# Kernel optimization log

Measured on AMD Instinct MI355X. Metric: run time of the kernel, lower is better.

Reference implementation:

```python
import jax, jax.numpy as jnp
import numpy as np

B, T, M, C, H = 4, 2048, 256, 512, 8
D = C // H  # head dim = 64


def _split_heads(t, n):  # [B,N,C] -> [B,H,N,D]
    b, s, c = t.shape
    return t.reshape(b, s, H, c // H).transpose(0, 2, 1, 3)


def setup_inputs() -> dict:
    key = jax.random.key(0)
    ks = jax.random.split(key, 16)
    s = 0.02
    inp = {
        "x": jax.random.normal(ks[0], (B, T, C), jnp.float32),
        "y": jax.random.normal(ks[1], (B, M, C), jnp.float32),
        "attn_x_mask": jnp.tril(jnp.ones((T, T), jnp.int32))[None, None],  # causal [1,1,T,T]
        "Wqkv_x": jax.random.normal(ks[2], (C, 3 * C), jnp.float32) * s,
        "bqkv_x": jnp.zeros((3 * C,), jnp.float32),
        "Wqkv_y": jax.random.normal(ks[3], (C, 3 * C), jnp.float32) * s,
        "bqkv_y": jnp.zeros((3 * C,), jnp.float32),
        "Wgs": jax.random.normal(ks[4], (C, C), jnp.float32) * s,
        "bgs": jnp.zeros((C,), jnp.float32),
        "Wgc": jax.random.normal(ks[5], (C, C), jnp.float32) * s,
        "bgc": jnp.zeros((C,), jnp.float32),
        "Wp": jax.random.normal(ks[6], (C, C), jnp.float32) * s,
        "bp": jnp.zeros((C,), jnp.float32),
    }
    return inp


def reference(x, y, attn_x_mask, Wqkv_x, bqkv_x, Wqkv_y, bqkv_y, Wgs, bgs, Wgc, bgc, Wp, bp):
    b, t, c = x.shape
    _, m, _ = y.shape
    scale = 1.0 / np.sqrt(D).astype(np.float32)

    qx, kx, vx = jnp.split(x @ Wqkv_x + bqkv_x, 3, axis=-1)
    qy, ky, vy = jnp.split(y @ Wqkv_y + bqkv_y, 3, axis=-1)
    qx, kx, vx = _split_heads(qx, H), _split_heads(kx, H), _split_heads(vx, H)
    qy, ky, vy = _split_heads(qy, H), _split_heads(ky, H), _split_heads(vy, H)

    # self-attn logits over x: [B,H,T,T]
    satt = jnp.einsum('bhtd,bhsd->bhts', qx, kx) * scale
    # cross scores y->x: [B,H,M,T]; bias = mean over M of softmax(dim=M)*scores -> [B,H,1,T]
    catt_y = jnp.einsum('bhmd,bhtd->bhmt', qy, kx) * scale
    bias = jnp.mean(jax.nn.softmax(catt_y, axis=-2) * catt_y, axis=-2, keepdims=True)
    satt = satt + bias  # broadcast over query rows
    satt = jnp.where(attn_x_mask == 0, -jnp.inf, satt)
    satt = jax.nn.softmax(satt, axis=-1)

    # cross-attn x->y: [B,H,T,M]
    catt = jax.nn.softmax(jnp.einsum('bhtd,bhmd->bhtm', qx, ky) * scale, axis=-1)

    sval = jnp.einsum('bhts,bhsd->bhtd', satt, vx).transpose(0, 2, 1, 3).reshape(b, t, c)
    cval = jnp.einsum('bhtm,bhmd->bhtd', catt, vy).transpose(0, 2, 1, 3).reshape(b, t, c)

    sgate = jax.nn.sigmoid(sval @ Wgs + bgs)
    cgate = jax.nn.sigmoid(cval @ Wgc + bgc)
    out = (sgate * cval + cgate * sval) @ Wp + bp
    return out
```

## Files before the change

### kernel.cpp

```cpp
#include <hip/hip_runtime.h>
#include <hip/hip_bf16.h>
#include <math.h>

#define B_ 4
#define T_ 2048
#define M_ 256
#define C_ 512
#define H_ 8
#define D_ 64
#define TC3 1536
#define QSCALE2 0.18033688f

typedef _Float16 half_t;
typedef _Float16 half8 __attribute__((ext_vector_type(8)));
typedef _Float16 half4 __attribute__((ext_vector_type(4)));
typedef float floatx4 __attribute__((ext_vector_type(4)));

__device__ __forceinline__ void gload_lds16(const half_t* g, half_t* lds) {
  __builtin_amdgcn_global_load_lds(
      (const __attribute__((address_space(1))) unsigned int*)g,
      (__attribute__((address_space(3))) unsigned int*)(unsigned)(unsigned long long)(void*)lds,
      16, 0, 0);
}

__device__ __forceinline__ floatx4 mfma16(half8 a, half8 b, floatx4 c) {
  return __builtin_amdgcn_mfma_f32_16x16x32_f16(a, b, c, 0, 0, 0);
}
__device__ __forceinline__ floatx4 mfma16k16(half4 a, half4 b, floatx4 c) {
  return __builtin_amdgcn_mfma_f32_16x16x16f16(a, b, c, 0, 0, 0);
}

__device__ __forceinline__ half8 frag64(const half_t* lds, int row, int kc, int quad) {
  int slot = ((kc << 2) + quad) ^ (row & 7);
  return *(const half8*)(lds + row * 64 + slot * 8);
}

__global__ __launch_bounds__(256) void conv_all(
    const float* x, half_t* xo, const float* y, half_t* yo,
    const float* w0, const float* w1, const float* w2, const float* w3, const float* w4,
    half_t* o0, half_t* o1, half_t* o2, half_t* o3, half_t* o4) {
  __shared__ float tile[32][33];
  const int tid = threadIdx.x;
  if (blockIdx.x < 2304) {
    int blk = blockIdx.x;
    const float* src; half_t* dst; int N;
    if (blk < 768)       { src = w0; dst = o0; N = 1536; }
    else if (blk < 1536) { src = w1; dst = o1; N = 1536; blk -= 768; }
    else if (blk < 1792) { src = w2; dst = o2; N = 512;  blk -= 1536; }
    else if (blk < 2048) { src = w3; dst = o3; N = 512;  blk -= 1792; }
    else                 { src = w4; dst = o4; N = 512;  blk -= 2048; }
    const int ntx = N >> 5;
    const int tk = blk / ntx, tn = blk % ntx;
    const int r = tid >> 3, c = (tid & 7) * 4;
    float4 v = *(const float4*)(src + (size_t)(tk * 32 + r) * N + tn * 32 + c);
    tile[r][c] = v.x; tile[r][c + 1] = v.y; tile[r][c + 2] = v.z; tile[r][c + 3] = v.w;
    __syncthreads();
    half4 h;
#pragma unroll
    for (int j = 0; j < 4; ++j) h[j] = (half_t)tile[c + j][r];
    *(half4*)(dst + (size_t)(tn * 32 + r) * 512 + tk * 32 + c) = h;
  } else {
    const int nx = B_ * T_ * C_, ny = B_ * M_ * C_;
    const int n4x = nx >> 2, tot = n4x + (ny >> 2);
    int i = (blockIdx.x - 2304) * 256 + tid;
    const int stride = (gridDim.x - 2304) * 256;
    for (; i < tot; i += stride) {
      const float4* s; half_t* d; int idx;
      if (i < n4x) { s = (const float4*)x; d = xo; idx = i; }
      else { s = (const float4*)y; d = yo; idx = i - n4x; }
      float4 v = s[idx];
      half4 h; h[0] = (half_t)v.x; h[1] = (half_t)v.y; h[2] = (half_t)v.z; h[3] = (half_t)v.w;
      *(half4*)(d + idx * 4) = h;
    }
  }
}

struct GemmAcc { floatx4 a[4][4]; };

__device__ __forceinline__ void gemm_core64(
    const half_t* __restrict__ A, const half_t* __restrict__ Wt,
    int rowBase, int colBase, GemmAcc& g,
    half_t* As, half_t* Bs, int tid) {
  const int lane = tid & 63, wave = tid >> 6;
  const int wm = wave >> 1, wn = wave & 1;
  const int qd = lane >> 4, lr = lane & 15;
  const int rr = lane >> 3, cc = lane & 7;
  const int cs = cc ^ rr;
#pragma unroll
  for (int mi = 0; mi < 4; ++mi)
#pragma unroll
    for (int ni = 0; ni < 4; ++ni)
#pragma unroll
      for (int r = 0; r < 4; ++r) g.a[mi][ni][r] = 0.f;
  for (int k0 = 0; k0 < 512; k0 += 64) {
    __syncthreads();
#pragma unroll
    for (int j = 0; j < 4; ++j) {
      int row = wave * 32 + j * 8 + rr;
      gload_lds16(A + (size_t)(rowBase + row) * 512 + k0 + cs * 8, As + (wave * 32 + j * 8) * 64);
      gload_lds16(Wt + (size_t)(colBase + row) * 512 + k0 + cs * 8, Bs + (wave * 32 + j * 8) * 64);
    }
    __syncthreads();
#pragma unroll
    for (int kc = 0; kc < 2; ++kc) {
      half8 af[4], bf[4];
#pragma unroll
      for (int mi = 0; mi < 4; ++mi) af[mi] = frag64(As, wm * 64 + mi * 16 + lr, kc, qd);
#pragma unroll
      for (int ni = 0; ni < 4; ++ni) bf[ni] = frag64(Bs, wn * 64 + ni * 16 + lr, kc, qd);
#pragma unroll
      for (int mi = 0; mi < 4; ++mi)
#pragma unroll
        for (int ni = 0; ni < 4; ++ni)
          g.a[mi][ni] = mfma16(af[mi], bf[ni], g.a[mi][ni]);
    }
  }
}

__global__ __launch_bounds__(256) void gemm_qkvt(
    const half_t* __restrict__ x16, const half_t* __restrict__ y16,
    const half_t* __restrict__ WxT, const half_t* __restrict__ WyT,
    const float* __restrict__ bqx, const float* __restrict__ bqy,
    half_t* __restrict__ qkvx, half_t* __restrict__ qkvy,
    half_t* __restrict__ vTx, half_t* __restrict__ vTy) {
  __shared__ __align__(16) half_t As[128 * 64];
  __shared__ __align__(16) half_t Bs[128 * 64];
  const int tid = threadIdx.x, lane = tid & 63, wave = tid >> 6;
  const int wm = wave >> 1, wn = wave & 1;
  const int qd = lane >> 4, lr = lane & 15;
  const int bxi = blockIdx.x;
  const half_t* A; const half_t* Wt; const float* bias; half_t* out;
  int rowBase, colBase, N; bool vt;
  if (bxi < 576) {
    vt = false; N = 1024;
    colBase = (bxi & 7) * 128;
    int ry = bxi >> 3;
    if (ry < 64) { A = x16; Wt = WxT; bias = bqx; out = qkvx; rowBase = ry * 128; }
    else { A = y16; Wt = WyT; bias = bqy; out = qkvy; rowBase = (ry - 64) * 128; }
  } else {
    vt = true;
    int i = bxi - 576;
    int xx = i % 18; int rest = i / 18;
    int yy = rest & 3, zz = rest >> 2;
    rowBase = yy * 128;
    if (xx < 16) {
      A = WxT + (size_t)1024 * 512; Wt = x16 + (size_t)zz * T_ * C_; bias = bqx + 1024;
      out = vTx + (size_t)zz * C_ * T_; N = T_; colBase = xx * 128;
    } else {
      A = WyT + (size_t)1024 * 512; Wt = y16 + (size_t)zz * M_ * C_; bias = bqy + 1024;
      out = vTy + (size_t)zz * C_ * M_; N = M_; colBase = (xx - 16) * 128;
    }
  }
  GemmAcc g;
  gemm_core64(A, Wt, rowBase, colBase, g, As, Bs, tid);
  if (!vt) {
#pragma unroll
    for (int ni = 0; ni < 4; ++ni) {
      int col = colBase + wn * 64 + ni * 16 + lr;
      float csc = (col < 512) ? QSCALE2 : 1.f;
      float bc = bias[col];
#pragma unroll
      for (int mi = 0; mi < 4; ++mi) {
        int row0 = rowBase + wm * 64 + mi * 16 + qd * 4;
#pragma unroll
        for (int r = 0; r < 4; ++r)
          out[(size_t)(row0 + r) * 1024 + col] = (half_t)((g.a[mi][ni][r] + bc) * csc);
      }
    }
  } else {
#pragma unroll
    for (int ni = 0; ni < 4; ++ni) {
      int col = colBase + wn * 64 + ni * 16 + lr;
#pragma unroll
      for (int mi = 0; mi < 4; ++mi) {
        int row0 = rowBase + wm * 64 + mi * 16 + qd * 4;
#pragma unroll
        for (int r = 0; r < 4; ++r)
          out[(size_t)(row0 + r) * N + col] = (half_t)(g.a[mi][ni][r] + bias[row0 + r]);
      }
    }
  }
}

__global__ __launch_bounds__(256) void bias_k(
    const half_t* __restrict__ qkvx, const half_t* __restrict__ qkvy,
    float* __restrict__ biasb) {
  __shared__ __align__(16) half_t Qy[256 * 64];
  __shared__ __align__(16) half_t Kx[128 * 64];
  const int tid = threadIdx.x, lane = tid & 63, wave = tid >> 6;
  const int bh = blockIdx.x >> 4;
  const int tb = (blockIdx.x & 15) * 128;
  const int b = bh >> 3, h = bh & 7;
  const int qd = lane >> 4, lr = lane & 15;
  const int rr = lane >> 3, cc = lane & 7;
  const int cs = cc ^ rr;
#pragma unroll
  for (int j = 0; j < 8; ++j) {
    int r = wave * 64 + j * 8 + rr;
    gload_lds16(qkvy + (size_t)(b * M_ + r) * 1024 + h * D_ + cs * 8,
                Qy + (wave * 64 + j * 8) * 64);
  }
#pragma unroll
  for (int j = 0; j < 4; ++j) {
    int r = wave * 32 + j * 8 + rr;
    gload_lds16(qkvx + (size_t)(b * T_ + tb + r) * 1024 + C_ + h * D_ + cs * 8,
                Kx + (wave * 32 + j * 8) * 64);
  }
  __syncthreads();
  half8 kf[2][2];
#pragma unroll
  for (int nt = 0; nt < 2; ++nt)
#pragma unroll
    for (int kc = 0; kc < 2; ++kc)
      kf[nt][kc] = frag64(Kx, wave * 32 + nt * 16 + lr, kc, qd);
  float ls[2] = {0.f, 0.f}, wsp[2] = {0.f, 0.f};
  for (int mt = 0; mt < 16; ++mt) {
    half8 af[2];
#pragma unroll
    for (int kc = 0; kc < 2; ++kc) af[kc] = frag64(Qy, mt * 16 + lr, kc, qd);
#pragma unroll
    for (int nt = 0; nt < 2; ++nt) {
      floatx4 s;
#pragma unroll
      for (int r = 0; r < 4; ++r) s[r] = 0.f;
#pragma unroll
      for (int kc = 0; kc < 2; ++kc) s = mfma16(af[kc], kf[nt][kc], s);
#pragma unroll
      for (int r = 0; r < 4; ++r) {
        float e = exp2f(s[r]);
        ls[nt] += e;
        wsp[nt] += e * s[r];
      }
    }
  }
#pragma unroll
  for (int nt = 0; nt < 2; ++nt) {
    ls[nt] += __shfl_xor(ls[nt], 16, 64);
    ls[nt] += __shfl_xor(ls[nt], 32, 64);
    wsp[nt] += __shfl_xor(wsp[nt], 16, 64);
    wsp[nt] += __shfl_xor(wsp[nt], 32, 64);
  }
  if (qd == 0) {
#pragma unroll
    for (int nt = 0; nt < 2; ++nt)
      biasb[bh * T_ + tb + wave * 32 + nt * 16 + lr] = wsp[nt] / (256.f * ls[nt]);
  }
}

template <bool USE_BIAS, bool DO_A, bool DIAG_A, bool DIAG_B>
__device__ __forceinline__ void attn_tile_dual(
    const half_t* __restrict__ Ks, const half_t* __restrict__ Vts,
    const float* __restrict__ Bsh, const half8* qfA, const half8* qfB,
    floatx4* oA, floatx4& lacA, floatx4* oB, floatx4& lacB,
    int qd, int lr, int thresh) {
  floatx4 sA[4], sB[4];
#pragma unroll
  for (int ks = 0; ks < 4; ++ks)
#pragma unroll
    for (int r = 0; r < 4; ++r) { sA[ks][r] = 0.f; sB[ks][r] = 0.f; }
#pragma unroll
  for (int kc = 0; kc < 2; ++kc) {
#pragma unroll
    for (int ks = 0; ks < 4; ++ks) {
      half8 kfr = frag64(Ks, ks * 16 + lr, kc, qd);
      if (DO_A) sA[ks] = mfma16(kfr, qfA[kc], sA[ks]);
      sB[ks] = mfma16(kfr, qfB[kc], sB[ks]);
    }
  }
  half4 pA[4], pB[4];
#pragma unroll
  for (int ks = 0; ks < 4; ++ks) {
    floatx4 bf;
    if (USE_BIAS) bf = *(const floatx4*)(Bsh + ks * 16 + qd * 4);
#pragma unroll
    for (int r = 0; r < 4; ++r) {
      int keyl = ks * 16 + qd * 4 + r;
      if (DO_A) {
        float t = USE_BIAS ? (sA[ks][r] + bf[r]) : sA[ks][r];
        float p1 = exp2f(t);
        if (DIAG_A && keyl > thresh) p1 = 0.f;
        pA[ks][r] = (half_t)p1;
      }
      float t2 = USE_BIAS ? (sB[ks][r] + bf[r]) : sB[ks][r];
      float p2 = exp2f(t2);
      if (DIAG_B && keyl > thresh) p2 = 0.f;
      pB[ks][r] = (half_t)p2;
    }
  }
  const half4 ones4 = {(half_t)1.f, (half_t)1.f, (half_t)1.f, (half_t)1.f};
#pragma unroll
  for (int ks = 0; ks < 4; ++ks) {
    int slot = (ks * 2 + (qd >> 1)) ^ (lr & 7);
    const half_t* vbase = Vts + slot * 8 + (qd & 1) * 4;
#pragma unroll
    for (int dt = 0; dt < 4; ++dt) {
      half4 vf = *(const half4*)(vbase + (dt * 16 + lr) * 64);
      if (DO_A) oA[dt] = mfma16k16(pA[ks], vf, oA[dt]);
      oB[dt] = mfma16k16(pB[ks], vf, oB[dt]);
    }
    if (DO_A) lacA = mfma16k16(pA[ks], ones4, lacA);
    lacB = mfma16k16(pB[ks], ones4, lacB);
  }
}

__device__ __forceinline__ void attn_step(
    int kt, int p, int ktEnd,
    const half_t* Ks, const half_t* Vts, const float* Bsh,
    const half8* qfA, const half8* qfB,
    floatx4* oA, floatx4& lacA, floatx4* oB, floatx4& lacB,
    int qd, int lr, int thresh) {
  if (kt < p)
    attn_tile_dual<true, true, false, false>(Ks, Vts, Bsh, qfA, qfB, oA, lacA, oB, lacB, qd, lr, thresh);
  else if (kt == p)
    attn_tile_dual<true, true, true, false>(Ks, Vts, Bsh, qfA, qfB, oA, lacA, oB, lacB, qd, lr, thresh);
  else if (kt < ktEnd)
    attn_tile_dual<true, false, false, false>(Ks, Vts, Bsh, qfA, qfB, oA, lacA, oB, lacB, qd, lr, thresh);
  else
    attn_tile_dual<true, false, false, true>(Ks, Vts, Bsh, qfA, qfB, oA, lacA, oB, lacB, qd, lr, thresh);
}

__device__ __forceinline__ void attn_store2(
    half_t* __restrict__ dst, const floatx4* o, floatx4 lac,
    int b, int qbase, int h, int qd, int lr) {
  floatx4 inv;
#pragma unroll
  for (int r = 0; r < 4; ++r) inv[r] = 1.f / lac[r];
#pragma unroll
  for (int dt = 0; dt < 4; ++dt)
#pragma unroll
    for (int r = 0; r < 4; ++r)
      dst[(size_t)(b * T_ + qbase + qd * 4 + r) * C_ + h * D_ + dt * 16 + lr] =
          (half_t)(o[dt][r] * inv[r]);
}

__global__ __launch_bounds__(256) void attn_fused(
    const half_t* __restrict__ qkvx, const half_t* __restrict__ qkvy,
    const half_t* __restrict__ vTx, const half_t* __restrict__ vTy,
    const float* __restrict__ biasb, half_t* __restrict__ sval,
    half_t* __restrict__ cval) {
  __shared__ __align__(16) half_t Qs[128 * 64];
  __shared__ __align__(16) half_t Ks[64 * 64];
  __shared__ __align__(16) half_t Vts[64 * 64];
  __shared__ __align__(16) float Bsh[64];
  const int tid = threadIdx.x, lane = tid & 63, wave = tid >> 6;
  const int qd = lane >> 4, lr = lane & 15;
  const int rr = lane >> 3, cc = lane & 7;
  const int cs = cc ^ rr;

  if (blockIdx.x < 512) {
    const int p = blockIdx.x & 15;
    const int bh = blockIdx.x >> 4;
    const int b = bh >> 3, h = bh & 7;
    const int qbL = p * 64, qbH = (31 - p) * 64;
#pragma unroll
    for (int j = 0; j < 4; ++j) {
      int rowIdx = wave * 32 + j * 8 + rr;
      int grow = (rowIdx < 64) ? (qbL + rowIdx) : (qbH + rowIdx - 64);
      gload_lds16(qkvx + (size_t)(b * T_ + grow) * 1024 + h * D_ + cs * 8,
                  Qs + (wave * 32 + j * 8) * 64);
    }
    __syncthreads();
    half8 qfA[2], qfB[2];
#pragma unroll
    for (int kc = 0; kc < 2; ++kc) {
      qfA[kc] = frag64(Qs, wave * 16 + lr, kc, qd);
      qfB[kc] = frag64(Qs, 64 + wave * 16 + lr, kc, qd);
    }
    floatx4 oA[4], oB[4], lacA, lacB;
#pragma unroll
    for (int dt = 0; dt < 4; ++dt)
#pragma unroll
      for (int r = 0; r < 4; ++r) { oA[dt][r] = 0.f; oB[dt][r] = 0.f; }
#pragma unroll
    for (int r = 0; r < 4; ++r) { lacA[r] = 0.f; lacB[r] = 0.f; }
    const int thresh = wave * 16 + lr;
    const int ktEnd = 31 - p;

    for (int kt = 0; kt <= ktEnd; ++kt) {
      const int kb = kt * 64;
      __syncthreads();
#pragma unroll
      for (int j = 0; j < 2; ++j) {
        int row = wave * 16 + j * 8 + rr;
        gload_lds16(qkvx + (size_t)(b * T_ + kb + row) * 1024 + C_ + h * D_ + cs * 8,
                    Ks + (wave * 16 + j * 8) * 64);
        gload_lds16(vTx + ((size_t)bh * 64 + row) * T_ + kb + cs * 8,
                    Vts + (wave * 16 + j * 8) * 64);
      }
      if (tid < 64) Bsh[tid] = biasb[bh * T_ + kb + tid];
      __syncthreads();
      attn_step(kt, p, ktEnd, Ks, Vts, Bsh, qfA, qfB, oA, lacA, oB, lacB, qd, lr, thresh);
    }
    attn_store2(sval, oA, lacA, b, qbL + wave * 16, h, qd, lr);
    attn_store2(sval, oB, lacB, b, qbH + wave * 16, h, qd, lr);
  } else {
    const int idx = blockIdx.x - 512;
    const int bh = idx >> 4;
    const int qb = (idx & 15) * 128;
    const int b = bh >> 3, h = bh & 7;
#pragma unroll
    for (int j = 0; j < 4; ++j) {
      int row = wave * 32 + j * 8 + rr;
      gload_lds16(qkvx + (size_t)(b * T_ + qb + row) * 1024 + h * D_ + cs * 8,
                  Qs + (wave * 32 + j * 8) * 64);
    }
    __syncthreads();
    half8 qfA[2], qfB[2];
#pragma unroll
    for (int kc = 0; kc < 2; ++kc) {
      qfA[kc] = frag64(Qs, wave * 32 + lr, kc, qd);
      qfB[kc] = frag64(Qs, wave * 32 + 16 + lr, kc, qd);
    }
    floatx4 oA[4], oB[4], lacA, lacB;
#pragma unroll
    for (int dt = 0; dt < 4; ++dt)
#pragma unroll
      for (int r = 0; r < 4; ++r) { oA[dt][r] = 0.f; oB[dt][r] = 0.f; }
#pragma unroll
    for (int r = 0; r < 4; ++r) { lacA[r] = 0.f; lacB[r] = 0.f; }

    for (int kt = 0; kt < 4; ++kt) {
      const int kb = kt * 64;
      __syncthreads();
#pragma unroll
      for (int j = 0; j < 2; ++j) {
        int row = wave * 16 + j * 8 + rr;
        gload_lds16(qkvy + (size_t)(b * M_ + kb + row) * 1024 + C_ + h * D_ + cs * 8,
                    Ks + (wave * 16 + j * 8) * 64);
        gload_lds16(vTy + ((size_t)bh * 64 + row) * M_ + kb + cs * 8,
                    Vts + (wave * 16 + j * 8) * 64);
      }
      __syncthreads();
      attn_tile_dual<false, true, false, false>(Ks, Vts, nullptr, qfA, qfB,
                                                oA, lacA, oB, lacB, qd, lr, 0);
    }
    attn_store2(cval, oA, lacA, b, qb + wave * 32, h, qd, lr);
    attn_store2(cval, oB, lacB, b, qb + wave * 32 + 16, h, qd, lr);
  }
}

__global__ __launch_bounds__(256) void gate_gemm64(
    const half_t* __restrict__ sv, const half_t* __restrict__ cv,
    const half_t* __restrict__ W1, const half_t* __restrict__ W2,
    const float* __restrict__ b1, const float* __restrict__ b2,
    half_t* __restrict__ z) {
  __shared__ __align__(16) half_t S1[64 * 64];
  __shared__ __align__(16) half_t S2[64 * 64];
  __shared__ __align__(16) half_t B1s[128 * 64];
  __shared__ __align__(16) half_t B2s[128 * 64];
  const int tid = threadIdx.x, lane = tid & 63, wave = tid >> 6;
  const int wm = wave >> 1, wn = wave & 1;
  const int rowBase = blockIdx.y * 64, colBase = blockIdx.x * 128;
  const int qd = lane >> 4, lr = lane & 15;
  const int rr = lane >> 3, cc = lane & 7;
  const int cs = cc ^ rr;

  floatx4 a1[2][4], a2[2][4];
#pragma unroll
  for (int mi = 0; mi < 2; ++mi)
#pragma unroll
    for (int ni = 0; ni < 4; ++ni)
#pragma unroll
      for (int r = 0; r < 4; ++r) { a1[mi][ni][r] = 0.f; a2[mi][ni][r] = 0.f; }

  for (int k0 = 0; k0 < 512; k0 += 64) {
    __syncthreads();
#pragma unroll
    for (int j = 0; j < 2; ++j) {
      int rA = wave * 16 + j * 8 + rr;
      gload_lds16(sv + (size_t)(rowBase + rA) * 512 + k0 + cs * 8, S1 + (wave * 16 + j * 8) * 64);
      gload_lds16(cv + (size_t)(rowBase + rA) * 512 + k0 + cs * 8, S2 + (wave * 16 + j * 8) * 64);
      gload_lds16(W1 + (size_t)(colBase + rA) * 512 + k0 + cs * 8, B1s + (wave * 16 + j * 8) * 64);
      gload_lds16(W1 + (size_t)(colBase + 64 + rA) * 512 + k0 + cs * 8, B1s + (64 + wave * 16 + j * 8) * 64);
      gload_lds16(W2 + (size_t)(colBase + rA) * 512 + k0 + cs * 8, B2s + (wave * 16 + j * 8) * 64);
      gload_lds16(W2 + (size_t)(colBase + 64 + rA) * 512 + k0 + cs * 8, B2s + (64 + wave * 16 + j * 8) * 64);
    }
    __syncthreads();
#pragma unroll
    for (int kc = 0; kc < 2; ++kc) {
      half8 af1[2], af2[2], bf1[4], bf2[4];
#pragma unroll
      for (int mi = 0; mi < 2; ++mi) {
        af1[mi] = frag64(S1, wm * 32 + mi * 16 + lr, kc, qd);
        af2[mi] = frag64(S2, wm * 32 + mi * 16 + lr, kc, qd);
      }
#pragma unroll
      for (int ni = 0; ni < 4; ++ni) {
        bf1[ni] = frag64(B1s, wn * 64 + ni * 16 + lr, kc, qd);
        bf2[ni] = frag64(B2s, wn * 64 + ni * 16 + lr, kc, qd);
      }
#pragma unroll
      for (int mi = 0; mi < 2; ++mi)
#pragma unroll
        for (int ni = 0; ni < 4; ++ni) {
          a1[mi][ni] = mfma16(af1[mi], bf1[ni], a1[mi][ni]);
          a2[mi][ni] = mfma16(af2[mi], bf2[ni], a2[mi][ni]);
        }
    }
  }

#pragma unroll
  for (int ni = 0; ni < 4; ++ni) {
    int col = colBase + wn * 64 + ni * 16 + lr;
    float g1b = b1[col], g2b = b2[col];
#pragma unroll
    for (int mi = 0; mi < 2; ++mi) {
      int row0 = rowBase + wm * 32 + mi * 16 + qd * 4;
#pragma unroll
      for (int r = 0; r < 4; ++r) {
        size_t idx = (size_t)(row0 + r) * 512 + col;
        float sg1 = 1.f / (1.f + __expf(-(a1[mi][ni][r] + g1b)));
        float sg2 = 1.f / (1.f + __expf(-(a2[mi][ni][r] + g2b)));
        z[idx] = (half_t)(sg1 * (float)cv[idx] + sg2 * (float)sv[idx]);
      }
    }
  }
}

__global__ __launch_bounds__(256) void gemm_final64(
    const half_t* __restrict__ A, const half_t* __restrict__ Wt,
    const float* __restrict__ bias, float* __restrict__ Cout) {
  __shared__ __align__(16) half_t As[64 * 64];
  __shared__ __align__(16) half_t Bs[128 * 64];
  const int tid = threadIdx.x, lane = tid & 63, wave = tid >> 6;
  const int wm = wave >> 1, wn = wave & 1;
  const int rowBase = blockIdx.y * 64, colBase = blockIdx.x * 128;
  const int qd = lane >> 4, lr = lane & 15;
  const int rr = lane >> 3, cc = lane & 7;
  const int cs = cc ^ rr;

  floatx4 acc[2][4];
#pragma unroll
  for (int mi = 0; mi < 2; ++mi)
#pragma unroll
    for (int ni = 0; ni < 4; ++ni)
#pragma unroll
      for (int r = 0; r < 4; ++r) acc[mi][ni][r] = 0.f;

  for (int k0 = 0; k0 < 512; k0 += 64) {
    __syncthreads();
#pragma unroll
    for (int j = 0; j < 2; ++j) {
      int rA = wave * 16 + j * 8 + rr;
      gload_lds16(A + (size_t)(rowBase + rA) * 512 + k0 + cs * 8, As + (wave * 16 + j * 8) * 64);
      gload_lds16(Wt + (size_t)(colBase + rA) * 512 + k0 + cs * 8, Bs + (wave * 16 + j * 8) * 64);
      gload_lds16(Wt + (size_t)(colBase + 64 + rA) * 512 + k0 + cs * 8, Bs + (64 + wave * 16 + j * 8) * 64);
    }
    __syncthreads();
#pragma unroll
    for (int kc = 0; kc < 2; ++kc) {
      half8 af[2], bf[4];
#pragma unroll
      for (int mi = 0; mi < 2; ++mi) af[mi] = frag64(As, wm * 32 + mi * 16 + lr, kc, qd);
#pragma unroll
      for (int ni = 0; ni < 4; ++ni) bf[ni] = frag64(Bs, wn * 64 + ni * 16 + lr, kc, qd);
#pragma unroll
      for (int mi = 0; mi < 2; ++mi)
#pragma unroll
        for (int ni = 0; ni < 4; ++ni)
          acc[mi][ni] = mfma16(af[mi], bf[ni], acc[mi][ni]);
    }
  }

#pragma unroll
  for (int ni = 0; ni < 4; ++ni) {
    int col = colBase + wn * 64 + ni * 16 + lr;
    float bc = bias[col];
#pragma unroll
    for (int mi = 0; mi < 2; ++mi) {
      int row0 = rowBase + wm * 32 + mi * 16 + qd * 4;
#pragma unroll
      for (int r = 0; r < 4; ++r)
        Cout[(size_t)(row0 + r) * 512 + col] = acc[mi][ni][r] + bc;
    }
  }
}

extern "C" void kernel_launch(void* const* d_in, const int* in_sizes, int n_in,
                              void* d_out, int out_size, void* d_ws, size_t ws_size,
                              hipStream_t stream) {
  (void)in_sizes; (void)n_in; (void)out_size; (void)ws_size;
  const float* x      = (const float*)d_in[0];
  const float* y      = (const float*)d_in[1];
  const float* Wqkv_x = (const float*)d_in[3];
  const float* bqkv_x = (const float*)d_in[4];
  const float* Wqkv_y = (const float*)d_in[5];
  const float* bqkv_y = (const float*)d_in[6];
  const float* Wgs    = (const float*)d_in[7];
  const float* bgs    = (const float*)d_in[8];
  const float* Wgc    = (const float*)d_in[9];
  const float* bgc    = (const float*)d_in[10];
  const float* Wp     = (const float*)d_in[11];
  const float* bp     = (const float*)d_in[12];
  float* out = (float*)d_out;

  half_t* h = (half_t*)d_ws;
  half_t* x16    = h;  h += (size_t)B_ * T_ * C_;
  half_t* y16    = h;  h += (size_t)B_ * M_ * C_;
  half_t* WqkvxT = h;  h += (size_t)TC3 * C_;
  half_t* WqkvyT = h;  h += (size_t)TC3 * C_;
  half_t* WgsT   = h;  h += (size_t)C_ * C_;
  half_t* WgcT   = h;  h += (size_t)C_ * C_;
  half_t* WpT    = h;  h += (size_t)C_ * C_;
  half_t* qkvx   = h;  h += (size_t)B_ * T_ * 1024;
  half_t* qkvy   = h;  h += (size_t)B_ * M_ * 1024;
  half_t* vTx    = h;  h += (size_t)B_ * C_ * T_;
  half_t* vTy    = h;  h += (size_t)B_ * C_ * M_;
  half_t* sval   = h;  h += (size_t)B_ * T_ * C_;
  half_t* cval   = h;  h += (size_t)B_ * T_ * C_;
  half_t* z      = h;  h += (size_t)B_ * T_ * C_;
  float* biasb   = (float*)h;

  conv_all<<<3456, 256, 0, stream>>>(x, x16, y, y16,
                                     Wqkv_x, Wqkv_y, Wgs, Wgc, Wp,
                                     WqkvxT, WqkvyT, WgsT, WgcT, WpT);

  gemm_qkvt<<<864, 256, 0, stream>>>(x16, y16, WqkvxT, WqkvyT,
                                     bqkv_x, bqkv_y, qkvx, qkvy, vTx, vTy);

  bias_k<<<512, 256, 0, stream>>>(qkvx, qkvy, biasb);

  attn_fused<<<1024, 256, 0, stream>>>(qkvx, qkvy, vTx, vTy, biasb, sval, cval);

  gate_gemm64<<<dim3(4, 128), 256, 0, stream>>>(sval, cval, WgsT, WgcT, bgs, bgc, z);

  gemm_final64<<<dim3(4, 128), 256, 0, stream>>>(z, WpT, bp, out);
}
```

Measured before the change: 238.8 us.

## Move cross-attention into bias kernel and split self-attention into its own launch

The bias computation and the cross-attention blocks now share one 1024-block launch, and self-attention runs as a separate 512-block kernel. The bias part loads Qy in two 128-row chunks so its shared memory stays at 32KB, the same as the cross-attention blocks. The aim is to balance the grid: cross-attention runs alongside the bias work instead of alongside the heavy causal self-attention blocks. The cost is an extra sync and reload step inside the bias blocks.

```diff
diff --git a/kernel.cpp b/kernel.cpp
--- a/kernel.cpp
+++ b/kernel.cpp
@@ -182,71 +182,6 @@
   }
 }
 
-__global__ __launch_bounds__(256) void bias_k(
-    const half_t* __restrict__ qkvx, const half_t* __restrict__ qkvy,
-    float* __restrict__ biasb) {
-  __shared__ __align__(16) half_t Qy[256 * 64];
-  __shared__ __align__(16) half_t Kx[128 * 64];
-  const int tid = threadIdx.x, lane = tid & 63, wave = tid >> 6;
-  const int bh = blockIdx.x >> 4;
-  const int tb = (blockIdx.x & 15) * 128;
-  const int b = bh >> 3, h = bh & 7;
-  const int qd = lane >> 4, lr = lane & 15;
-  const int rr = lane >> 3, cc = lane & 7;
-  const int cs = cc ^ rr;
-#pragma unroll
-  for (int j = 0; j < 8; ++j) {
-    int r = wave * 64 + j * 8 + rr;
-    gload_lds16(qkvy + (size_t)(b * M_ + r) * 1024 + h * D_ + cs * 8,
-                Qy + (wave * 64 + j * 8) * 64);
-  }
-#pragma unroll
-  for (int j = 0; j < 4; ++j) {
-    int r = wave * 32 + j * 8 + rr;
-    gload_lds16(qkvx + (size_t)(b * T_ + tb + r) * 1024 + C_ + h * D_ + cs * 8,
-                Kx + (wave * 32 + j * 8) * 64);
-  }
-  __syncthreads();
-  half8 kf[2][2];
-#pragma unroll
-  for (int nt = 0; nt < 2; ++nt)
-#pragma unroll
-    for (int kc = 0; kc < 2; ++kc)
-      kf[nt][kc] = frag64(Kx, wave * 32 + nt * 16 + lr, kc, qd);
-  float ls[2] = {0.f, 0.f}, wsp[2] = {0.f, 0.f};
-  for (int mt = 0; mt < 16; ++mt) {
-    half8 af[2];
-#pragma unroll
-    for (int kc = 0; kc < 2; ++kc) af[kc] = frag64(Qy, mt * 16 + lr, kc, qd);
-#pragma unroll
-    for (int nt = 0; nt < 2; ++nt) {
-      floatx4 s;
-#pragma unroll
-      for (int r = 0; r < 4; ++r) s[r] = 0.f;
-#pragma unroll
-      for (int kc = 0; kc < 2; ++kc) s = mfma16(af[kc], kf[nt][kc], s);
-#pragma unroll
-      for (int r = 0; r < 4; ++r) {
-        float e = exp2f(s[r]);
-        ls[nt] += e;
-        wsp[nt] += e * s[r];
-      }
-    }
-  }
-#pragma unroll
-  for (int nt = 0; nt < 2; ++nt) {
-    ls[nt] += __shfl_xor(ls[nt], 16, 64);
-    ls[nt] += __shfl_xor(ls[nt], 32, 64);
-    wsp[nt] += __shfl_xor(wsp[nt], 16, 64);
-    wsp[nt] += __shfl_xor(wsp[nt], 32, 64);
-  }
-  if (qd == 0) {
-#pragma unroll
-    for (int nt = 0; nt < 2; ++nt)
-      biasb[bh * T_ + tb + wave * 32 + nt * 16 + lr] = wsp[nt] / (256.f * ls[nt]);
-  }
-}
-
 template <bool USE_BIAS, bool DO_A, bool DIAG_A, bool DIAG_B>
 __device__ __forceinline__ void attn_tile_dual(
     const half_t* __restrict__ Ks, const half_t* __restrict__ Vts,
@@ -333,67 +268,143 @@
           (half_t)(o[dt][r] * inv[r]);
 }
 
-__global__ __launch_bounds__(256) void attn_fused(
-    const half_t* __restrict__ qkvx, const half_t* __restrict__ qkvy,
-    const half_t* __restrict__ vTx, const half_t* __restrict__ vTy,
-    const float* __restrict__ biasb, half_t* __restrict__ sval,
-    half_t* __restrict__ cval) {
+__global__ __launch_bounds__(256) void self_attn_reg(
+    const half_t* __restrict__ qkv, const half_t* __restrict__ vT,
+    const float* __restrict__ biasb, half_t* __restrict__ sval) {
   __shared__ __align__(16) half_t Qs[128 * 64];
   __shared__ __align__(16) half_t Ks[64 * 64];
   __shared__ __align__(16) half_t Vts[64 * 64];
   __shared__ __align__(16) float Bsh[64];
   const int tid = threadIdx.x, lane = tid & 63, wave = tid >> 6;
+  const int p = blockIdx.x & 15;
+  const int bh = blockIdx.x >> 4;
+  const int b = bh >> 3, h = bh & 7;
+  const int qbL = p * 64, qbH = (31 - p) * 64;
   const int qd = lane >> 4, lr = lane & 15;
   const int rr = lane >> 3, cc = lane & 7;
   const int cs = cc ^ rr;
 
+#pragma unroll
+  for (int j = 0; j < 4; ++j) {
+    int rowIdx = wave * 32 + j * 8 + rr;
+    int grow = (rowIdx < 64) ? (qbL + rowIdx) : (qbH + rowIdx - 64);
+    gload_lds16(qkv + (size_t)(b * T_ + grow) * 1024 + h * D_ + cs * 8,
+                Qs + (wave * 32 + j * 8) * 64);
+  }
+  __syncthreads();
+  half8 qfA[2], qfB[2];
+#pragma unroll
+  for (int kc = 0; kc < 2; ++kc) {
+    qfA[kc] = frag64(Qs, wave * 16 + lr, kc, qd);
+    qfB[kc] = frag64(Qs, 64 + wave * 16 + lr, kc, qd);
+  }
+  floatx4 oA[4], oB[4], lacA, lacB;
+#pragma unroll
+  for (int dt = 0; dt < 4; ++dt)
+#pragma unroll
+    for (int r = 0; r < 4; ++r) { oA[dt][r] = 0.f; oB[dt][r] = 0.f; }
+#pragma unroll
+  for (int r = 0; r < 4; ++r) { lacA[r] = 0.f; lacB[r] = 0.f; }
+  const int thresh = wave * 16 + lr;
+  const int ktEnd = 31 - p;
+
+  for (int kt = 0; kt <= ktEnd; ++kt) {
+    const int kb = kt * 64;
+    __syncthreads();
+#pragma unroll
+    for (int j = 0; j < 2; ++j) {
+      int row = wave * 16 + j * 8 + rr;
+      gload_lds16(qkv + (size_t)(b * T_ + kb + row) * 1024 + C_ + h * D_ + cs * 8,
+                  Ks + (wave * 16 + j * 8) * 64);
+      gload_lds16(vT + ((size_t)bh * 64 + row) * T_ + kb + cs * 8,
+                  Vts + (wave * 16 + j * 8) * 64);
+    }
+    if (tid < 64) Bsh[tid] = biasb[bh * T_ + kb + tid];
+    __syncthreads();
+    attn_step(kt, p, ktEnd, Ks, Vts, Bsh, qfA, qfB, oA, lacA, oB, lacB, qd, lr, thresh);
+  }
+  attn_store2(sval, oA, lacA, b, qbL + wave * 16, h, qd, lr);
+  attn_store2(sval, oB, lacB, b, qbH + wave * 16, h, qd, lr);
+}
+
+__global__ __launch_bounds__(256) void bias_cross(
+    const half_t* __restrict__ qkvx, const half_t* __restrict__ qkvy,
+    const half_t* __restrict__ vTy, float* __restrict__ biasb,
+    half_t* __restrict__ cval) {
+  __shared__ __align__(16) half_t smem[16384];
+  const int tid = threadIdx.x, lane = tid & 63, wave = tid >> 6;
+  const int qd = lane >> 4, lr = lane & 15;
+  const int rr = lane >> 3, cc = lane & 7;
+  const int cs = cc ^ rr;
   if (blockIdx.x < 512) {
-    const int p = blockIdx.x & 15;
+    half_t* Qy = smem;
+    half_t* Kx = smem + 8192;
     const int bh = blockIdx.x >> 4;
+    const int tb = (blockIdx.x & 15) * 128;
     const int b = bh >> 3, h = bh & 7;
-    const int qbL = p * 64, qbH = (31 - p) * 64;
 #pragma unroll
     for (int j = 0; j < 4; ++j) {
-      int rowIdx = wave * 32 + j * 8 + rr;
-      int grow = (rowIdx < 64) ? (qbL + rowIdx) : (qbH + rowIdx - 64);
-      gload_lds16(qkvx + (size_t)(b * T_ + grow) * 1024 + h * D_ + cs * 8,
-                  Qs + (wave * 32 + j * 8) * 64);
-    }
-    __syncthreads();
-    half8 qfA[2], qfB[2];
-#pragma unroll
-    for (int kc = 0; kc < 2; ++kc) {
-      qfA[kc] = frag64(Qs, wave * 16 + lr, kc, qd);
-      qfB[kc] = frag64(Qs, 64 + wave * 16 + lr, kc, qd);
-    }
-    floatx4 oA[4], oB[4], lacA, lacB;
-#pragma unroll
-    for (int dt = 0; dt < 4; ++dt)
-#pragma unroll
-      for (int r = 0; r < 4; ++r) { oA[dt][r] = 0.f; oB[dt][r] = 0.f; }
-#pragma unroll
-    for (int r = 0; r < 4; ++r) { lacA[r] = 0.f; lacB[r] = 0.f; }
-    const int thresh = wave * 16 + lr;
-    const int ktEnd = 31 - p;
-
-    for (int kt = 0; kt <= ktEnd; ++kt) {
-      const int kb = kt * 64;
-      __syncthreads();
-#pragma unroll
-      for (int j = 0; j < 2; ++j) {
-        int row = wave * 16 + j * 8 + rr;
-        gload_lds16(qkvx + (size_t)(b * T_ + kb + row) * 1024 + C_ + h * D_ + cs * 8,
-                    Ks + (wave * 16 + j * 8) * 64);
-        gload_lds16(vTx + ((size_t)bh * 64 + row) * T_ + kb + cs * 8,
-                    Vts + (wave * 16 + j * 8) * 64);
-      }
-      if (tid < 64) Bsh[tid] = biasb[bh * T_ + kb + tid];
-      __syncthreads();
-      attn_step(kt, p, ktEnd, Ks, Vts, Bsh, qfA, qfB, oA, lacA, oB, lacB, qd, lr, thresh);
-    }
-    attn_store2(sval, oA, lacA, b, qbL + wave * 16, h, qd, lr);
-    attn_store2(sval, oB, lacB, b, qbH + wave * 16, h, qd, lr);
+      int r = wave * 32 + j * 8 + rr;
+      gload_lds16(qkvx + (size_t)(b * T_ + tb + r) * 1024 + C_ + h * D_ + cs * 8,
+                  Kx + (wave * 32 + j * 8) * 64);
+      gload_lds16(qkvy + (size_t)(b * M_ + r) * 1024 + h * D_ + cs * 8,
+                  Qy + (wave * 32 + j * 8) * 64);
+    }
+    __syncthreads();
+    half8 kf[2][2];
+#pragma unroll
+    for (int nt = 0; nt < 2; ++nt)
+#pragma unroll
+      for (int kc = 0; kc < 2; ++kc)
+        kf[nt][kc] = frag64(Kx, wave * 32 + nt * 16 + lr, kc, qd);
+    float ls[2] = {0.f, 0.f}, wsp[2] = {0.f, 0.f};
+    for (int chunk = 0; chunk < 2; ++chunk) {
+      if (chunk) {
+        __syncthreads();
+#pragma unroll
+        for (int j = 0; j < 4; ++j) {
+          int r = wave * 32 + j * 8 + rr;
+          gload_lds16(qkvy + (size_t)(b * M_ + 128 + r) * 1024 + h * D_ + cs * 8,
+                      Qy + (wave * 32 + j * 8) * 64);
+        }
+        __syncthreads();
+      }
+      for (int mt = 0; mt < 8; ++mt) {
+        half8 af[2];
+#pragma unroll
+        for (int kc = 0; kc < 2; ++kc) af[kc] = frag64(Qy, mt * 16 + lr, kc, qd);
+#pragma unroll
+        for (int nt = 0; nt < 2; ++nt) {
+          floatx4 s;
+#pragma unroll
+          for (int r = 0; r < 4; ++r) s[r] = 0.f;
+#pragma unroll
+          for (int kc = 0; kc < 2; ++kc) s = mfma16(af[kc], kf[nt][kc], s);
+#pragma unroll
+          for (int r = 0; r < 4; ++r) {
+            float e = exp2f(s[r]);
+            ls[nt] += e;
+            wsp[nt] += e * s[r];
+          }
+        }
+      }
+    }
+#pragma unroll
+    for (int nt = 0; nt < 2; ++nt) {
+      ls[nt] += __shfl_xor(ls[nt], 16, 64);
+      ls[nt] += __shfl_xor(ls[nt], 32, 64);
+      wsp[nt] += __shfl_xor(wsp[nt], 16, 64);
+      wsp[nt] += __shfl_xor(wsp[nt], 32, 64);
+    }
+    if (qd == 0) {
+#pragma unroll
+      for (int nt = 0; nt < 2; ++nt)
+        biasb[bh * T_ + tb + wave * 32 + nt * 16 + lr] = wsp[nt] / (256.f * ls[nt]);
+    }
   } else {
+    half_t* Qs  = smem;
+    half_t* Ks  = smem + 8192;
+    half_t* Vts = smem + 12288;
     const int idx = blockIdx.x - 512;
     const int bh = idx >> 4;
     const int qb = (idx & 15) * 128;
@@ -418,7 +429,6 @@
       for (int r = 0; r < 4; ++r) { oA[dt][r] = 0.f; oB[dt][r] = 0.f; }
 #pragma unroll
     for (int r = 0; r < 4; ++r) { lacA[r] = 0.f; lacB[r] = 0.f; }
-
     for (int kt = 0; kt < 4; ++kt) {
       const int kb = kt * 64;
       __syncthreads();
@@ -618,9 +628,9 @@
   gemm_qkvt<<<864, 256, 0, stream>>>(x16, y16, WqkvxT, WqkvyT,
                                      bqkv_x, bqkv_y, qkvx, qkvy, vTx, vTy);
 
-  bias_k<<<512, 256, 0, stream>>>(qkvx, qkvy, biasb);
-
-  attn_fused<<<1024, 256, 0, stream>>>(qkvx, qkvy, vTx, vTy, biasb, sval, cval);
+  bias_cross<<<1024, 256, 0, stream>>>(qkvx, qkvy, vTy, biasb, cval);
+
+  self_attn_reg<<<512, 256, 0, stream>>>(qkvx, vTx, biasb, sval);
 
   gate_gemm64<<<dim3(4, 128), 256, 0, stream>>>(sval, cval, WgsT, WgcT, bgs, bgc, z);
 
```

Result: no change. 241.2 us (+1.0%).
